# Kernel optimization log

Hardware: AMD Instinct MI355X
Metric: run time of the kernel (lower is better)

The kernel has to match this reference:

```python
import jax, jax.numpy as jnp
import numpy as np

BS, S, D, H, KVH, HD = 2, 2048, 2048, 32, 8, 64
N_REP = H // KVH
N_DOCS = 4


def setup_inputs() -> dict:
    key = jax.random.key(0)
    ks = jax.random.split(key, 7)
    x = jax.random.normal(ks[0], (BS, S, D), dtype=jnp.float32)
    # RoPE table (llama theta=10000), stored as real (cos, sin) pairs: [S, HD//2, 2]
    inv_freq = 1.0 / (10000.0 ** (jnp.arange(0, HD, 2, dtype=jnp.float32) / HD))
    ang = jnp.arange(S, dtype=jnp.float32)[:, None] * inv_freq[None, :]  # [S, HD//2]
    freqs_cis = jnp.stack([jnp.cos(ang), jnp.sin(ang)], axis=-1)
    # packed-document ids, non-decreasing along sequence: [BS, S]
    sequence_id = jnp.sort(
        jax.random.randint(ks[1], (BS, S), 0, N_DOCS, dtype=jnp.int32), axis=-1
    )
    std = 0.02
    wq = jax.random.normal(ks[2], (H * HD, D), dtype=jnp.float32) * std
    wk = jax.random.normal(ks[3], (KVH * HD, D), dtype=jnp.float32) * std
    wv = jax.random.normal(ks[4], (KVH * HD, D), dtype=jnp.float32) * std
    wo = jax.random.normal(ks[5], (D, H * HD), dtype=jnp.float32) * std
    return {"x": x, "freqs_cis": freqs_cis, "sequence_id": sequence_id,
            "wq": wq, "wk": wk, "wv": wv, "wo": wo}


def _apply_rope(t, freqs_cis):
    # t: [b, s, h, hd]; freqs_cis: [s, hd//2, 2] (cos, sin)
    b, s, h, hd = t.shape
    tp = t.reshape(b, s, h, hd // 2, 2)
    t0, t1 = tp[..., 0], tp[..., 1]
    cos = freqs_cis[None, :, None, :, 0]
    sin = freqs_cis[None, :, None, :, 1]
    o0 = t0 * cos - t1 * sin
    o1 = t0 * sin + t1 * cos
    return jnp.stack([o0, o1], axis=-1).reshape(b, s, h, hd)


def reference(x, freqs_cis, sequence_id, wq, wk, wv, wo):
    bs, s, _ = x.shape
    xq = (x @ wq.T).reshape(bs, s, H, HD)
    xk = (x @ wk.T).reshape(bs, s, KVH, HD)
    xv = (x @ wv.T).reshape(bs, s, KVH, HD)
    xq = _apply_rope(xq, freqs_cis)
    xk = _apply_rope(xk, freqs_cis)
    # GQA without materializing repeated KV: group queries by kv head
    q = xq.reshape(bs, s, KVH, N_REP, HD).transpose(0, 2, 3, 1, 4)  # [b,g,r,s,d]
    k = xk.transpose(0, 2, 1, 3)  # [b,g,s,d]
    v = xv.transpose(0, 2, 1, 3)  # [b,g,s,d]
    scale = 1.0 / jnp.sqrt(jnp.float32(HD))
    scores = jnp.einsum("bgrqd,bgkd->bgrqk", q, k) * scale
    # document-causal mask: same sequence_id AND causal
    causal = jnp.tril(jnp.ones((s, s), dtype=bool))
    same_doc = sequence_id[:, :, None] == sequence_id[:, None, :]  # [b,s,s]
    mask = (causal[None] & same_doc)[:, None, None, :, :]  # [b,1,1,s,s]
    scores = jnp.where(mask, scores, jnp.float32(-1e30))
    probs = jax.nn.softmax(scores, axis=-1)
    out = jnp.einsum("bgrqk,bgkd->bgrqd", probs, v)  # [b,g,r,s,d]
    out = out.transpose(0, 3, 1, 2, 4).reshape(bs, s, H * HD)
    return out @ wo.T
```

## Files before the change

### kernel.cpp

```cpp
#include <hip/hip_runtime.h>
#include <hip/hip_bf16.h>

typedef __attribute__((ext_vector_type(8))) short bf16x8;
typedef __attribute__((ext_vector_type(4))) float f32x4;

#define MFMA16(A, B, C) __builtin_amdgcn_mfma_f32_16x16x32_bf16(A, B, C, 0, 0, 0)

__device__ __forceinline__ unsigned short f2bf(float f) {
    unsigned int u = __float_as_uint(f);
    u += 0x7fffu + ((u >> 16) & 1u);
    return (unsigned short)(u >> 16);
}
__device__ __forceinline__ float bf2f(unsigned short h) {
    return __uint_as_float(((unsigned int)h) << 16);
}
__device__ __forceinline__ unsigned int pack_bf2(float lo, float hi) {
    __hip_bfloat162 h = __float22bfloat162_rn(make_float2(lo, hi));
    return *reinterpret_cast<unsigned int*>(&h);
}

__device__ __forceinline__ void gload_lds16(const void* g, void* l) {
    __builtin_amdgcn_global_load_lds(
        (__attribute__((address_space(1))) unsigned int*)g,
        (__attribute__((address_space(3))) unsigned int*)l, 16, 0, 0);
}

__device__ __forceinline__ int swz128(int by) {
    return by ^ (((by >> 7) & 7) << 4);
}

__global__ void cvt_kernel(const float* __restrict__ in, unsigned short* __restrict__ out, int n4) {
    const int i = blockIdx.x * 256 + threadIdx.x;
    if (i >= n4) return;
    const float4 v = ((const float4*)in)[i];
    uint2 o;
    o.x = pack_bf2(v.x, v.y);
    o.y = pack_bf2(v.z, v.w);
    ((uint2*)out)[i] = o;
}

__global__ void docstart_kernel(const int* __restrict__ sid, int* __restrict__ ds) {
    const int i = blockIdx.x * 256 + threadIdx.x;
    const int b = i >> 11, s = i & 2047;
    const int* row = sid + b * 2048;
    const int v = row[s];
    int lo = 0, hi = s;
    while (lo < hi) { const int mid = (lo + hi) >> 1; if (row[mid] < v) lo = mid + 1; else hi = mid; }
    ds[i] = lo;
}

#define QKV_K 2048
#define QKV_NT 32
__global__ __launch_bounds__(512, 2) void gemm_qkv8(
    const unsigned short* __restrict__ A,
    const unsigned short* __restrict__ B,
    unsigned short* __restrict__ oq,
    unsigned short* __restrict__ ok,
    unsigned short* __restrict__ ov)
{
    __shared__ __align__(16) unsigned short S[2][2][2][8192];
    const int tid = threadIdx.x, lane = tid & 63, w = tid >> 6;
    const int wr = w >> 2, wc = w & 3;
    const int lr = lane & 15, lc = lane >> 4;

    int bid = blockIdx.x;
    bid = (bid & 7) * 24 + (bid >> 3);
    const int m0 = (bid / 12) * 256, n0 = (bid % 12) * 256;

    const int o0 = (w << 11) + (lane << 4);
    const int o1 = o0 + 1024;
    const int v0 = swz128(o0);
    const int v1 = swz128(o1);
    const int r0 = v0 >> 7, c0 = (v0 & 127) >> 1;
    const int r1 = v1 >> 7, c1 = (v1 & 127) >> 1;
    const size_t aoff0 = (size_t)(m0 + r0) * QKV_K + c0;
    const size_t aoff1 = (size_t)(m0 + r1) * QKV_K + c1;
    const size_t boff0 = (size_t)(n0 + r0) * QKV_K + c0;
    const size_t boff1 = (size_t)(n0 + r1) * QKV_K + c1;
    const int d0 = o0 >> 1, d1 = o1 >> 1;

    f32x4 acc[2][2][4][2];
#pragma unroll
    for (int a = 0; a < 2; a++)
#pragma unroll
        for (int bq = 0; bq < 2; bq++)
#pragma unroll
            for (int i = 0; i < 4; i++)
#pragma unroll
                for (int j = 0; j < 2; j++) acc[a][bq][i][j] = (f32x4){0.f, 0.f, 0.f, 0.f};

    bf16x8 Af[4][2], Bf0[2][2], Bf1[2][2];

    auto STAGE_A = [&](int bf, int h, int kt) {
        gload_lds16(A + aoff0 + (size_t)h * 128 * QKV_K + (size_t)kt * 64, &S[bf][0][h][d0]);
        gload_lds16(A + aoff1 + (size_t)h * 128 * QKV_K + (size_t)kt * 64, &S[bf][0][h][d1]);
    };
    auto STAGE_B = [&](int bf, int h, int kt) {
        gload_lds16(B + boff0 + (size_t)h * 128 * QKV_K + (size_t)kt * 64, &S[bf][1][h][d0]);
        gload_lds16(B + boff1 + (size_t)h * 128 * QKV_K + (size_t)kt * 64, &S[bf][1][h][d1]);
    };
    auto LDA = [&](int bf, int mh) {
#pragma unroll
        for (int i = 0; i < 4; i++)
#pragma unroll
            for (int kh = 0; kh < 2; kh++) {
                const int by = swz128(((wr * 64 + i * 16 + lr) << 7) + (kh << 6) + (lc << 4));
                Af[i][kh] = *(const bf16x8*)((const char*)&S[bf][0][mh][0] + by);
            }
    };
    auto LDB = [&](int bf, int nh, bf16x8 (&Bf)[2][2]) {
#pragma unroll
        for (int j = 0; j < 2; j++)
#pragma unroll
            for (int kh = 0; kh < 2; kh++) {
                const int by = swz128(((wc * 32 + j * 16 + lr) << 7) + (kh << 6) + (lc << 4));
                Bf[j][kh] = *(const bf16x8*)((const char*)&S[bf][1][nh][0] + by);
            }
    };
    auto QUAD = [&](f32x4 (&ac)[4][2], bf16x8 (&Bf)[2][2]) {
        __builtin_amdgcn_s_setprio(1);
#pragma unroll
        for (int i = 0; i < 4; i++)
#pragma unroll
            for (int j = 0; j < 2; j++)
#pragma unroll
                for (int kh = 0; kh < 2; kh++)
                    ac[i][j] = MFMA16(Af[i][kh], Bf[j][kh], ac[i][j]);
        __builtin_amdgcn_s_setprio(0);
    };

#define BAR() __builtin_amdgcn_s_barrier()
#define LGKM0() asm volatile("s_waitcnt lgkmcnt(0)" ::: "memory")

    STAGE_A(0, 0, 0); STAGE_A(0, 1, 0); STAGE_B(0, 0, 0); STAGE_B(0, 1, 0);
    STAGE_A(1, 0, 1); STAGE_B(1, 1, 1); STAGE_A(1, 1, 1);
    asm volatile("s_waitcnt vmcnt(6)" ::: "memory");
    BAR();

    auto GROUP = [&](int g, int bf) {
        LDA(bf, 0); LDB(bf, 0, Bf0);
        if (g + 1 < QKV_NT) STAGE_B(bf ^ 1, 0, g + 1);
        BAR(); LGKM0();
        QUAD(acc[0][0], Bf0);
        BAR();
        LDB(bf, 1, Bf1);
        if (g + 2 < QKV_NT) STAGE_A(bf, 0, g + 2);
        BAR(); LGKM0();
        QUAD(acc[0][1], Bf1);
        BAR();
        LDA(bf, 1);
        if (g + 2 < QKV_NT) STAGE_B(bf, 1, g + 2);
        BAR(); LGKM0();
        QUAD(acc[1][1], Bf1);
        BAR();
        if (g + 2 < QKV_NT) STAGE_A(bf, 1, g + 2);
        BAR();
        QUAD(acc[1][0], Bf0);
        if (g == QKV_NT - 2) { asm volatile("s_waitcnt vmcnt(0)" ::: "memory"); }
        else                 { asm volatile("s_waitcnt vmcnt(6)" ::: "memory"); }
        BAR();
    };

#pragma unroll 1
    for (int g = 0; g < QKV_NT; g += 2) {
        GROUP(g, 0);
        GROUP(g + 1, 1);
    }

#pragma unroll
    for (int mh = 0; mh < 2; mh++)
#pragma unroll
        for (int nh = 0; nh < 2; nh++)
#pragma unroll
            for (int i = 0; i < 4; i++)
#pragma unroll
                for (int j = 0; j < 2; j++) {
                    const int n = n0 + nh * 128 + wc * 32 + j * 16 + lr;
                    const int d = n & 63;
                    const int hh6 = n >> 6;
#pragma unroll
                    for (int r = 0; r < 4; r++) {
                        const int m = m0 + mh * 128 + wr * 64 + i * 16 + lc * 4 + r;
                        const int bb = m >> 11, s = m & 2047;
                        const unsigned short val = f2bf(acc[mh][nh][i][j][r]);
                        if (n < 2048) {
                            oq[((((size_t)bb * 32 + hh6) * 2048 + s) << 6) + d] = val;
                        } else if (n < 2560) {
                            ok[((((size_t)bb * 8 + (hh6 - 32)) * 2048 + s) << 6) + d] = val;
                        } else {
                            ov[((((size_t)bb * 8 + (hh6 - 40)) * 2048 + s) << 6) + d] = val;
                        }
                    }
                }
}
#undef BAR
#undef LGKM0

template <int EPI>
__global__ __launch_bounds__(256) void gemm_bt(
    const unsigned short* __restrict__ A,
    const unsigned short* __restrict__ B,
    int K, int N,
    unsigned short* __restrict__ oq,
    unsigned short* __restrict__ ok,
    unsigned short* __restrict__ ov,
    float* __restrict__ of)
{
    __shared__ __align__(16) unsigned short sA[128 * 32];
    __shared__ __align__(16) unsigned short sB[128 * 32];
    const int tid = threadIdx.x;
    const int lane = tid & 63, wave = tid >> 6;
    const int wr = wave >> 1, wc = wave & 1;
    const int lr = lane & 15, lc = lane >> 4;

    int bid = blockIdx.y * gridDim.x + blockIdx.x;
    const int cpx = (gridDim.x * gridDim.y) >> 3;
    bid = (bid & 7) * cpx + (bid >> 3);
    const int m0 = (bid / gridDim.x) * 128, n0 = (bid % gridDim.x) * 128;

    f32x4 acc[4][4];
#pragma unroll
    for (int i = 0; i < 4; i++)
#pragma unroll
        for (int j = 0; j < 4; j++) acc[i][j] = (f32x4){0.f, 0.f, 0.f, 0.f};

    const int u0 = tid, u1 = tid + 256;
    for (int k0 = 0; k0 < K; k0 += 32) {
        __syncthreads();
        gload_lds16(A + (size_t)(m0 + (u0 >> 2)) * K + k0 + (u0 & 3) * 8, &sA[u0 * 8]);
        gload_lds16(A + (size_t)(m0 + (u1 >> 2)) * K + k0 + (u1 & 3) * 8, &sA[u1 * 8]);
        gload_lds16(B + (size_t)(n0 + (u0 >> 2)) * K + k0 + (u0 & 3) * 8, &sB[u0 * 8]);
        gload_lds16(B + (size_t)(n0 + (u1 >> 2)) * K + k0 + (u1 & 3) * 8, &sB[u1 * 8]);
        __syncthreads();
        bf16x8 af[4], bfv[4];
#pragma unroll
        for (int i = 0; i < 4; i++) {
            af[i]  = *(const bf16x8*)&sA[(wr * 64 + i * 16 + lr) * 32 + lc * 8];
            bfv[i] = *(const bf16x8*)&sB[(wc * 64 + i * 16 + lr) * 32 + lc * 8];
        }
#pragma unroll
        for (int i = 0; i < 4; i++)
#pragma unroll
            for (int j = 0; j < 4; j++) acc[i][j] = MFMA16(af[i], bfv[j], acc[i][j]);
    }

    if (EPI == 0) {
#pragma unroll
        for (int i = 0; i < 4; i++) {
#pragma unroll
            for (int j = 0; j < 4; j++) {
                const int n = n0 + wc * 64 + j * 16 + lr;
                const int d = n & 63;
#pragma unroll
                for (int r = 0; r < 4; r++) {
                    const int m = m0 + wr * 64 + i * 16 + lc * 4 + r;
                    const int bb = m >> 11, s = m & 2047;
                    const unsigned short val = f2bf(acc[i][j][r]);
                    if (n < 2048) {
                        const int hh = n >> 6;
                        oq[((((size_t)bb * 32 + hh) * 2048 + s) << 6) + d] = val;
                    } else if (n < 2560) {
                        const int hh = (n >> 6) - 32;
                        ok[((((size_t)bb * 8 + hh) * 2048 + s) << 6) + d] = val;
                    } else {
                        const int hh = (n >> 6) - 40;
                        ov[((((size_t)bb * 8 + hh) * 2048 + s) << 6) + d] = val;
                    }
                }
            }
        }
    } else {
#pragma unroll
        for (int i = 0; i < 4; i++)
#pragma unroll
            for (int j = 0; j < 4; j++)
#pragma unroll
                for (int r = 0; r < 4; r++) {
                    const int m = m0 + wr * 64 + i * 16 + lc * 4 + r;
                    const int n = n0 + wc * 64 + j * 16 + lr;
                    of[(size_t)m * N + n] = acc[i][j][r];
                }
    }
}

__global__ void rope_kernel(unsigned short* __restrict__ Qb,
                            unsigned short* __restrict__ Kb,
                            const float* __restrict__ fc)
{
    const int NQ = 2 * 32 * 2048 * 32;
    int i = blockIdx.x * 256 + threadIdx.x;
    unsigned short* base;
    if (i < NQ) base = Qb;
    else { base = Kb; i -= NQ; }
    const int p = i & 31, s = (i >> 5) & 2047, bh = i >> 16;
    const size_t off = (((size_t)bh * 2048 + s) << 6) + p * 2;
    const unsigned int w = *(const unsigned int*)&base[off];
    const float t0 = bf2f((unsigned short)(w & 0xffffu));
    const float t1 = bf2f((unsigned short)(w >> 16));
    const float c = fc[(s * 32 + p) * 2], sn = fc[(s * 32 + p) * 2 + 1];
    *(unsigned int*)&base[off] = pack_bf2(t0 * c - t1 * sn, t0 * sn + t1 * c);
}

__global__ __launch_bounds__(256) void attn_kernel(
    const unsigned short* __restrict__ Q,
    const unsigned short* __restrict__ K,
    const unsigned short* __restrict__ V,
    const int* __restrict__ dstart,
    unsigned short* __restrict__ AO)
{
    const int qt = 31 - blockIdx.x;
    const int h = blockIdx.y, b = blockIdx.z;
    const int kvh = h >> 2;
    const int tid = threadIdx.x, lane = tid & 63, wave = tid >> 6;
    const int lr = lane & 15, lc = lane >> 4;
    const int q0 = qt * 64;
    const int qw = q0 + wave * 16;

    __shared__ __align__(16) unsigned short sK[64 * 64];
    __shared__ __align__(16) unsigned short sVt[64][72];

    const unsigned short* Qh = Q + (((size_t)b * 32 + h) * 2048) * 64;
    const unsigned short* Kh = K + (((size_t)b * 8 + kvh) * 2048) * 64;
    const unsigned short* Vh = V + (((size_t)b * 8 + kvh) * 2048) * 64;

    const bf16x8 qf0 = *(const bf16x8*)&Qh[(size_t)(qw + lr) * 64 + lc * 8];
    const bf16x8 qf1 = *(const bf16x8*)&Qh[(size_t)(qw + lr) * 64 + 32 + lc * 8];

    const int qglob = qw + lr;
    const int dsl = dstart[b * 2048 + qglob];
    const int ds_wmin = dstart[b * 2048 + qw];
    const int t0 = dstart[b * 2048 + q0] & ~63;

    float mrow = -1e30f, lrow = 0.f;
    f32x4 oacc[4];
#pragma unroll
    for (int j = 0; j < 4; j++) oacc[j] = (f32x4){0.f, 0.f, 0.f, 0.f};

    for (int t = t0; t < q0 + 64; t += 64) {
        __syncthreads();
        {
            int slot = tid;
            int r = slot >> 3, c = slot & 7;
            gload_lds16(Kh + (size_t)(t + r) * 64 + ((c ^ (r & 7)) * 8), &sK[slot * 8]);
            slot = tid + 256; r = slot >> 3; c = slot & 7;
            gload_lds16(Kh + (size_t)(t + r) * 64 + ((c ^ (r & 7)) * 8), &sK[slot * 8]);
        }
        {
            const int w8 = wave * 8;
            const uint4 va = *(const uint4*)&Vh[(size_t)(t + lane) * 64 + w8];
            const uint4 vb = *(const uint4*)&Vh[(size_t)(t + lane) * 64 + 32 + w8];
            const unsigned short* pa = (const unsigned short*)&va;
            const unsigned short* pb = (const unsigned short*)&vb;
#pragma unroll
            for (int e = 0; e < 8; e++) sVt[w8 + e][lane] = pa[e];
#pragma unroll
            for (int e = 0; e < 8; e++) sVt[32 + w8 + e][lane] = pb[e];
        }
        asm volatile("s_waitcnt vmcnt(0)" ::: "memory");
        __syncthreads();
        if (t > qw + 15 || t + 63 < ds_wmin) continue;

        f32x4 sc[4];
#pragma unroll
        for (int kk = 0; kk < 4; kk++) {
            const int krow = kk * 16 + lr;
            const bf16x8 kf0 = *(const bf16x8*)&sK[krow * 64 + ((lc ^ (lr & 7)) * 8)];
            const bf16x8 kf1 = *(const bf16x8*)&sK[krow * 64 + (((4 + lc) ^ (lr & 7)) * 8)];
            f32x4 a = (f32x4){0.f, 0.f, 0.f, 0.f};
            a = MFMA16(kf0, qf0, a);
            a = MFMA16(kf1, qf1, a);
            sc[kk] = a;
        }
        float vmax = -3e38f;
#pragma unroll
        for (int kk = 0; kk < 4; kk++)
#pragma unroll
            for (int r = 0; r < 4; r++) {
                const int kpos = t + kk * 16 + lc * 4 + r;
                const bool okm = (kpos <= qglob) && (kpos >= dsl);
                sc[kk][r] = okm ? sc[kk][r] * 0.125f : -3e38f;
                vmax = fmaxf(vmax, sc[kk][r]);
            }
        vmax = fmaxf(vmax, __shfl_xor(vmax, 16));
        vmax = fmaxf(vmax, __shfl_xor(vmax, 32));
        const float mnew = fmaxf(mrow, vmax);
        const float corr = __expf(mrow - mnew);
        mrow = mnew;

        float rsum = 0.f;
        unsigned int pk[4][2];
#pragma unroll
        for (int kk = 0; kk < 4; kk++) {
            const float p0 = __expf(sc[kk][0] - mnew);
            const float p1 = __expf(sc[kk][1] - mnew);
            const float p2 = __expf(sc[kk][2] - mnew);
            const float p3 = __expf(sc[kk][3] - mnew);
            rsum += (p0 + p1) + (p2 + p3);
            pk[kk][0] = pack_bf2(p0, p1);
            pk[kk][1] = pack_bf2(p2, p3);
        }
        rsum += __shfl_xor(rsum, 16);
        rsum += __shfl_xor(rsum, 32);
        lrow = lrow * corr + rsum;
#pragma unroll
        for (int j = 0; j < 4; j++)
#pragma unroll
            for (int r = 0; r < 4; r++) oacc[j][r] *= corr;

        const int srcEven = 32 * (lc & 1) + lr;
        const int srcOdd  = srcEven + 16;
        const bool hiKK = (lc & 2) != 0;
        union { unsigned int w[4]; bf16x8 v; } B0, B1;
        {
            unsigned int a, c;
            a = __shfl(pk[0][0], srcEven); c = __shfl(pk[1][0], srcEven); B0.w[0] = hiKK ? c : a;
            a = __shfl(pk[0][1], srcEven); c = __shfl(pk[1][1], srcEven); B0.w[1] = hiKK ? c : a;
            a = __shfl(pk[0][0], srcOdd);  c = __shfl(pk[1][0], srcOdd);  B0.w[2] = hiKK ? c : a;
            a = __shfl(pk[0][1], srcOdd);  c = __shfl(pk[1][1], srcOdd);  B0.w[3] = hiKK ? c : a;
            a = __shfl(pk[2][0], srcEven); c = __shfl(pk[3][0], srcEven); B1.w[0] = hiKK ? c : a;
            a = __shfl(pk[2][1], srcEven); c = __shfl(pk[3][1], srcEven); B1.w[1] = hiKK ? c : a;
            a = __shfl(pk[2][0], srcOdd);  c = __shfl(pk[3][0], srcOdd);  B1.w[2] = hiKK ? c : a;
            a = __shfl(pk[2][1], srcOdd);  c = __shfl(pk[3][1], srcOdd);  B1.w[3] = hiKK ? c : a;
        }

#pragma unroll
        for (int j = 0; j < 4; j++) {
            const bf16x8 a0 = *(const bf16x8*)&sVt[j * 16 + lr][lc * 8];
            const bf16x8 a1 = *(const bf16x8*)&sVt[j * 16 + lr][32 + lc * 8];
            oacc[j] = MFMA16(a0, B0.v, oacc[j]);
            oacc[j] = MFMA16(a1, B1.v, oacc[j]);
        }
    }

    __syncthreads();
    const float inv = 1.0f / lrow;
#pragma unroll
    for (int j = 0; j < 4; j++)
#pragma unroll
        for (int p = 0; p < 2; p++) {
            const unsigned int w = pack_bf2(oacc[j][2 * p] * inv, oacc[j][2 * p + 1] * inv);
            *(unsigned int*)&sVt[wave * 16 + lr][j * 16 + lc * 4 + 2 * p] = w;
        }
    __syncthreads();
#pragma unroll
    for (int half = 0; half < 2; half++) {
        const int c = lane + 64 * half;
        const int row = c >> 3, ch = c & 7;
        const uint4 o = *(const uint4*)&sVt[wave * 16 + row][ch * 8];
        *(uint4*)&AO[((size_t)b * 2048 + qw + row) * 2048 + h * 64 + ch * 8] = o;
    }
}

extern "C" void kernel_launch(void* const* d_in, const int* in_sizes, int n_in,
                              void* d_out, int out_size, void* d_ws, size_t ws_size,
                              hipStream_t stream) {
    const float* x  = (const float*)d_in[0];
    const float* fc = (const float*)d_in[1];
    const int* sid  = (const int*)d_in[2];
    const float* wq = (const float*)d_in[3];
    const float* wk = (const float*)d_in[4];
    const float* wv = (const float*)d_in[5];
    const float* wo = (const float*)d_in[6];
    float* out = (float*)d_out;

    unsigned short* xb   = (unsigned short*)d_ws;
    unsigned short* wqkv = xb + (size_t)4096 * 2048;
    unsigned short* wob  = wqkv + (size_t)3072 * 2048;
    unsigned short* Qb   = wob + (size_t)2048 * 2048;
    unsigned short* Kb   = Qb + (size_t)2 * 32 * 2048 * 64;
    unsigned short* Vb   = Kb + (size_t)2 * 8 * 2048 * 64;
    unsigned short* AO   = Vb + (size_t)2 * 8 * 2048 * 64;
    int* dstart = (int*)(AO + (size_t)4096 * 2048);

    cvt_kernel<<<8192, 256, 0, stream>>>(x, xb, 2097152);
    cvt_kernel<<<4096, 256, 0, stream>>>(wq, wqkv, 1048576);
    cvt_kernel<<<1024, 256, 0, stream>>>(wk, wqkv + (size_t)2048 * 2048, 262144);
    cvt_kernel<<<1024, 256, 0, stream>>>(wv, wqkv + (size_t)2560 * 2048, 262144);
    cvt_kernel<<<4096, 256, 0, stream>>>(wo, wob, 1048576);
    docstart_kernel<<<16, 256, 0, stream>>>(sid, dstart);
    gemm_qkv8<<<dim3(192), 512, 0, stream>>>(xb, wqkv, Qb, Kb, Vb);
    rope_kernel<<<20480, 256, 0, stream>>>(Qb, Kb, fc);
    attn_kernel<<<dim3(32, 32, 2), 256, 0, stream>>>(Qb, Kb, Vb, dstart, AO);
    gemm_bt<1><<<dim3(16, 32), 256, 0, stream>>>(AO, wob, 2048, 2048, nullptr, nullptr, nullptr, out);
}
```

Baseline: 209.4 us.

## Restructure QKV GEMM main loop into two-phase pipeline with inline-asm LDS reads

Rewrites the fused QKV GEMM main loop as two phases per k-tile instead of four quarter-steps. Each phase issues all B fragments plus the next A half through hand-written ds_read_b128 with precomputed swizzled immediate offsets. Prefetching the next tile's A half overlaps LDS reads with MFMA, and the number of barriers and full lgkmcnt(0) waits drops. The cost is more live fragment registers, and the partial vmcnt/lgkmcnt counts must exactly match the issue order or results will be wrong.

Measured after the change: 241.7 us. +15.5%, slower.

```diff
diff --git a/kernel.cpp b/kernel.cpp
--- a/kernel.cpp
+++ b/kernel.cpp
@@ -51,6 +51,35 @@
 
 #define QKV_K 2048
 #define QKV_NT 32
+
+#define DSR(dst, addr, IMM) \
+    asm volatile("ds_read_b128 %0, %1 offset:" #IMM : "=v"(dst) : "v"(addr))
+#define VMW(N) asm volatile("s_waitcnt vmcnt(" #N ")" ::: "memory")
+#define LGW(N) do { asm volatile("s_waitcnt lgkmcnt(" #N ")" ::: "memory"); \
+                    __builtin_amdgcn_sched_barrier(0); } while (0)
+#define BAR() __builtin_amdgcn_s_barrier()
+
+#define READ_B8(bb0, bb1) do { \
+    DSR(Br[0][0][0], bb0, 0);     DSR(Br[0][0][1], bb1, 0); \
+    DSR(Br[0][1][0], bb0, 2048);  DSR(Br[0][1][1], bb1, 2048); \
+    DSR(Br[1][0][0], bb0, 16384); DSR(Br[1][0][1], bb1, 16384); \
+    DSR(Br[1][1][0], bb0, 18432); DSR(Br[1][1][1], bb1, 18432); \
+} while (0)
+
+#define READ_A8_H0(Ar, ab0, ab1) do { \
+    DSR(Ar[0][0], ab0, 0);     DSR(Ar[0][1], ab1, 0); \
+    DSR(Ar[1][0], ab0, 2048);  DSR(Ar[1][1], ab1, 2048); \
+    DSR(Ar[2][0], ab0, 4096);  DSR(Ar[2][1], ab1, 4096); \
+    DSR(Ar[3][0], ab0, 6144);  DSR(Ar[3][1], ab1, 6144); \
+} while (0)
+
+#define READ_A8_H1(Ar, ab0, ab1) do { \
+    DSR(Ar[0][0], ab0, 16384); DSR(Ar[0][1], ab1, 16384); \
+    DSR(Ar[1][0], ab0, 18432); DSR(Ar[1][1], ab1, 18432); \
+    DSR(Ar[2][0], ab0, 20480); DSR(Ar[2][1], ab1, 20480); \
+    DSR(Ar[3][0], ab0, 22528); DSR(Ar[3][1], ab1, 22528); \
+} while (0)
+
 __global__ __launch_bounds__(512, 2) void gemm_qkv8(
     const unsigned short* __restrict__ A,
     const unsigned short* __restrict__ B,
@@ -69,8 +98,7 @@
 
     const int o0 = (w << 11) + (lane << 4);
     const int o1 = o0 + 1024;
-    const int v0 = swz128(o0);
-    const int v1 = swz128(o1);
+    const int v0 = swz128(o0), v1 = swz128(o1);
     const int r0 = v0 >> 7, c0 = (v0 & 127) >> 1;
     const int r1 = v1 >> 7, c1 = (v1 & 127) >> 1;
     const size_t aoff0 = (size_t)(m0 + r0) * QKV_K + c0;
@@ -79,6 +107,14 @@
     const size_t boff1 = (size_t)(n0 + r1) * QKV_K + c1;
     const int d0 = o0 >> 1, d1 = o1 >> 1;
 
+    const unsigned sbase =
+        (unsigned)(size_t)(__attribute__((address_space(3))) unsigned short*)&S[0][0][0][0];
+    const int sw = (lr & 7) << 4;
+    const int arow = (wr * 64 + lr) << 7;
+    const int brow = (wc * 32 + lr) << 7;
+    const int xk0 = (lc << 4) ^ sw;
+    const int xk1 = (64 | (lc << 4)) ^ sw;
+
     f32x4 acc[2][2][4][2];
 #pragma unroll
     for (int a = 0; a < 2; a++)
@@ -89,7 +125,7 @@
 #pragma unroll
                 for (int j = 0; j < 2; j++) acc[a][bq][i][j] = (f32x4){0.f, 0.f, 0.f, 0.f};
 
-    bf16x8 Af[4][2], Bf0[2][2], Bf1[2][2];
+    bf16x8 A0r[4][2], A1r[4][2], Br[2][2][2];
 
     auto STAGE_A = [&](int bf, int h, int kt) {
         gload_lds16(A + aoff0 + (size_t)h * 128 * QKV_K + (size_t)kt * 64, &S[bf][0][h][d0]);
@@ -99,72 +135,58 @@
         gload_lds16(B + boff0 + (size_t)h * 128 * QKV_K + (size_t)kt * 64, &S[bf][1][h][d0]);
         gload_lds16(B + boff1 + (size_t)h * 128 * QKV_K + (size_t)kt * 64, &S[bf][1][h][d1]);
     };
-    auto LDA = [&](int bf, int mh) {
-#pragma unroll
-        for (int i = 0; i < 4; i++)
-#pragma unroll
-            for (int kh = 0; kh < 2; kh++) {
-                const int by = swz128(((wr * 64 + i * 16 + lr) << 7) + (kh << 6) + (lc << 4));
-                Af[i][kh] = *(const bf16x8*)((const char*)&S[bf][0][mh][0] + by);
-            }
-    };
-    auto LDB = [&](int bf, int nh, bf16x8 (&Bf)[2][2]) {
-#pragma unroll
-        for (int j = 0; j < 2; j++)
-#pragma unroll
-            for (int kh = 0; kh < 2; kh++) {
-                const int by = swz128(((wc * 32 + j * 16 + lr) << 7) + (kh << 6) + (lc << 4));
-                Bf[j][kh] = *(const bf16x8*)((const char*)&S[bf][1][nh][0] + by);
-            }
-    };
-    auto QUAD = [&](f32x4 (&ac)[4][2], bf16x8 (&Bf)[2][2]) {
+    auto MFMA_HALF = [&](f32x4 (&ac)[2][4][2], bf16x8 (&Ar)[4][2]) {
         __builtin_amdgcn_s_setprio(1);
 #pragma unroll
-        for (int i = 0; i < 4; i++)
-#pragma unroll
-            for (int j = 0; j < 2; j++)
-#pragma unroll
-                for (int kh = 0; kh < 2; kh++)
-                    ac[i][j] = MFMA16(Af[i][kh], Bf[j][kh], ac[i][j]);
+        for (int nh = 0; nh < 2; nh++)
+#pragma unroll
+            for (int i = 0; i < 4; i++)
+#pragma unroll
+                for (int j = 0; j < 2; j++)
+#pragma unroll
+                    for (int kh = 0; kh < 2; kh++)
+                        ac[nh][i][j] = MFMA16(Ar[i][kh], Br[nh][j][kh], ac[nh][i][j]);
         __builtin_amdgcn_s_setprio(0);
     };
 
-#define BAR() __builtin_amdgcn_s_barrier()
-#define LGKM0() asm volatile("s_waitcnt lgkmcnt(0)" ::: "memory")
-
-    STAGE_A(0, 0, 0); STAGE_A(0, 1, 0); STAGE_B(0, 0, 0); STAGE_B(0, 1, 0);
-    STAGE_A(1, 0, 1); STAGE_B(1, 1, 1); STAGE_A(1, 1, 1);
-    asm volatile("s_waitcnt vmcnt(6)" ::: "memory");
-    BAR();
-
-    auto GROUP = [&](int g, int bf) {
-        LDA(bf, 0); LDB(bf, 0, Bf0);
-        if (g + 1 < QKV_NT) STAGE_B(bf ^ 1, 0, g + 1);
-        BAR(); LGKM0();
-        QUAD(acc[0][0], Bf0);
+    STAGE_A(0, 0, 0); STAGE_B(0, 0, 0);
+    STAGE_B(0, 1, 0); STAGE_A(0, 1, 0);
+    STAGE_A(1, 0, 1); STAGE_B(1, 0, 1);
+    VMW(8);
+    {
+        const unsigned ab0 = sbase + arow + xk0;
+        const unsigned ab1 = sbase + arow + xk1;
+        READ_A8_H0(A0r, ab0, ab1);
+    }
+
+#pragma unroll 1
+    for (int g = 0; g < QKV_NT; ++g) {
+        const int bf = g & 1;
+        const unsigned ab0 = sbase + (bf << 16) + arow + xk0;
+        const unsigned ab1 = sbase + (bf << 16) + arow + xk1;
+        const unsigned bb0 = sbase + (bf << 16) + 32768 + brow + xk0;
+        const unsigned bb1 = sbase + (bf << 16) + 32768 + brow + xk1;
+
         BAR();
-        LDB(bf, 1, Bf1);
-        if (g + 2 < QKV_NT) STAGE_A(bf, 0, g + 2);
-        BAR(); LGKM0();
-        QUAD(acc[0][1], Bf1);
+        if (g == QKV_NT - 1) { VMW(0); } else { VMW(4); }
+        if (g + 1 < QKV_NT) { STAGE_B(bf ^ 1, 1, g + 1); STAGE_A(bf ^ 1, 1, g + 1); }
+        READ_B8(bb0, bb1);
+        READ_A8_H1(A1r, ab0, ab1);
+        LGW(8);
+        MFMA_HALF(acc[0], A0r);
+
         BAR();
-        LDA(bf, 1);
-        if (g + 2 < QKV_NT) STAGE_B(bf, 1, g + 2);
-        BAR(); LGKM0();
-        QUAD(acc[1][1], Bf1);
-        BAR();
-        if (g + 2 < QKV_NT) STAGE_A(bf, 1, g + 2);
-        BAR();
-        QUAD(acc[1][0], Bf0);
-        if (g == QKV_NT - 2) { asm volatile("s_waitcnt vmcnt(0)" ::: "memory"); }
-        else                 { asm volatile("s_waitcnt vmcnt(6)" ::: "memory"); }
-        BAR();
-    };
-
-#pragma unroll 1
-    for (int g = 0; g < QKV_NT; g += 2) {
-        GROUP(g, 0);
-        GROUP(g + 1, 1);
+        if (g + 2 < QKV_NT) { STAGE_A(bf, 0, g + 2); STAGE_B(bf, 0, g + 2); }
+        if (g + 1 < QKV_NT) {
+            if (g == QKV_NT - 2) { VMW(4); } else { VMW(8); }
+            const unsigned nab0 = sbase + ((bf ^ 1) << 16) + arow + xk0;
+            const unsigned nab1 = sbase + ((bf ^ 1) << 16) + arow + xk1;
+            READ_A8_H0(A0r, nab0, nab1);
+            LGW(8);
+        } else {
+            LGW(0);
+        }
+        MFMA_HALF(acc[1], A1r);
     }
 
 #pragma unroll
@@ -193,8 +215,6 @@
                     }
                 }
 }
-#undef BAR
-#undef LGKM0
 
 template <int EPI>
 __global__ __launch_bounds__(256) void gemm_bt(
```
